# Kernel optimization log

Hardware: AMD Instinct MI355X
Metric: run time of the kernel (lower is better)

The kernel has to match this reference:

```python
import jax, jax.numpy as jnp
import numpy as np

N_PROTS, D = 20000, 256
N_NODES, N_EDGES = 100000, 320000
N_GRAPHS, OUT = 64, 978
EPS = 1e-5


def setup_inputs() -> dict:
    key = jax.random.key(0)
    ks = jax.random.split(key, 24)
    f = jax.random.normal
    inp = {
        'global_idx': jax.random.randint(ks[0], (N_NODES,), 0, N_PROTS),
        'acts': f(ks[1], (N_NODES, 2), dtype=jnp.float32),
        'edge_index': jax.random.randint(ks[2], (2, N_EDGES), 0, N_NODES),
        'sign': f(ks[3], (N_EDGES, 2), dtype=jnp.float32),
        'batch': jnp.sort(jax.random.randint(ks[4], (N_NODES,), 0, N_GRAPHS)),
        # parameters
        'emb_weight': f(ks[5], (N_PROTS, D)) * 0.02,
        'pe_W': f(ks[6], (2, D)) * 0.02,
        'pe_b': jnp.zeros((D,)),
        'cg_Wf': f(ks[7], (2 * D + 2, D)) * 0.02,
        'cg_bf': jnp.zeros((D,)),
        'cg_Ws': f(ks[8], (2 * D + 2, D)) * 0.02,
        'cg_bs': jnp.zeros((D,)),
        'gat_W': f(ks[9], (4, D, D)) * 0.05,
        'gat_att_src': f(ks[10], (4, D)) * 0.05,
        'gat_att_dst': f(ks[11], (4, D)) * 0.05,
        'gat_bias': jnp.zeros((4, D)),
        'bn_gamma': jnp.ones((5, D)),
        'bn_beta': jnp.zeros((5, D)),
        'prelu_alpha': jnp.full((5,), 0.25),
        'fc1_W': f(ks[12], (D, 2 * D)) * 0.02,
        'fc1_b': jnp.zeros((2 * D,)),
        'fc2_W': f(ks[13], (2 * D, OUT)) * 0.02,
        'fc2_b': jnp.zeros((OUT,)),
    }
    return inp


def _bn(h, gamma, beta):
    # eval-mode BatchNorm1d with running_mean=0, running_var=1
    return h / jnp.sqrt(1.0 + EPS) * gamma + beta


def _prelu(h, a):
    return jnp.where(h >= 0, h, a * h)


def _cgconv(x, src, dst, sign, Wf, bf, Ws, bs):
    # PyG CGConv: z = [x_i, x_j, e_ij]; out = x + sum_j sigmoid(lin_f(z)) * softplus(lin_s(z))
    z = jnp.concatenate([x[dst], x[src], sign], axis=-1)  # [E, 2D+2]
    msg = jax.nn.sigmoid(z @ Wf + bf) * jax.nn.softplus(z @ Ws + bs)
    return x + jax.ops.segment_sum(msg, dst, num_segments=x.shape[0])


def _gat(x, src_sl, dst_sl, W, a_src, a_dst, b):
    # PyG GATConv, heads=1, self-loops already appended to src_sl/dst_sl
    N = x.shape[0]
    h = x @ W                                  # [N, D]
    asrc = h @ a_src                           # [N]
    adst = h @ a_dst                           # [N]
    logit = jax.nn.leaky_relu(asrc[src_sl] + adst[dst_sl], 0.2)  # [E+N]
    m = jax.ops.segment_max(logit, dst_sl, num_segments=N)
    ex = jnp.exp(logit - m[dst_sl])
    denom = jax.ops.segment_sum(ex, dst_sl, num_segments=N)
    coef = ex / denom[dst_sl]
    out = jax.ops.segment_sum(h[src_sl] * coef[:, None], dst_sl, num_segments=N)
    return out + b


def reference(global_idx, acts, edge_index, sign, batch, emb_weight, pe_W, pe_b,
              cg_Wf, cg_bf, cg_Ws, cg_bs, gat_W, gat_att_src, gat_att_dst,
              gat_bias, bn_gamma, bn_beta, prelu_alpha, fc1_W, fc1_b, fc2_W, fc2_b):
    N = global_idx.shape[0]
    src, dst = edge_index[0], edge_index[1]
    loop = jnp.arange(N)
    src_sl = jnp.concatenate([src, loop])
    dst_sl = jnp.concatenate([dst, loop])

    x = emb_weight[global_idx] + (acts @ pe_W + pe_b)

    h = _cgconv(x, src, dst, sign, cg_Wf, cg_bf, cg_Ws, cg_bs)
    h = _prelu(_bn(h, bn_gamma[0], bn_beta[0]) + x, prelu_alpha[0])

    for l in range(4):
        g = _gat(h, src_sl, dst_sl, gat_W[l], gat_att_src[l], gat_att_dst[l], gat_bias[l])
        h = _prelu(_bn(g, bn_gamma[l + 1], bn_beta[l + 1]) + h, prelu_alpha[l + 1])

    # NOTE: original code pools the *input* features x (x is never reassigned
    # to x_5 before pooling) -- reproduced faithfully.
    pooled = jax.ops.segment_sum(x, batch, num_segments=N_GRAPHS)  # [G, D]
    z = jax.nn.relu(pooled @ fc1_W + fc1_b)
    return jax.nn.log_softmax(z @ fc2_W + fc2_b, axis=-1)
```

## Files before the change

kernel.cpp:

```cpp
#include <hip/hip_runtime.h>


#define NNODES  100000
#define NGRAPHS 64
#define DIM     256
#define HID     512
#define NOUT    978
#define NPW     32

__global__ __launch_bounds__(256) void pool_k(
    const int* __restrict__ gidx, const float* __restrict__ acts,
    const int* __restrict__ batch, const float* __restrict__ emb,
    const float* __restrict__ peW, const float* __restrict__ peb,
    float* __restrict__ pooled)
{
    const int wave = blockIdx.x * 4 + (threadIdx.x >> 6);
    const int lane = threadIdx.x & 63;
    const int start = wave * NPW;
    if (start >= NNODES) return;

    const float4 w0 = ((const float4*)peW)[lane];
    const float4 w1 = ((const float4*)(peW + DIM))[lane];
    const float4 pb = ((const float4*)peb)[lane];

    float4 acc  = make_float4(0.f, 0.f, 0.f, 0.f);
    float2 asum = make_float2(0.f, 0.f);
    float  cnt  = 0.f;
    int cur = batch[start];

    auto flush = [&]() {
        float* p = pooled + (size_t)cur * DIM + lane * 4;
        atomicAdd(p + 0, acc.x + asum.x * w0.x + asum.y * w1.x + cnt * pb.x);
        atomicAdd(p + 1, acc.y + asum.x * w0.y + asum.y * w1.y + cnt * pb.y);
        atomicAdd(p + 2, acc.z + asum.x * w0.z + asum.y * w1.z + cnt * pb.z);
        atomicAdd(p + 3, acc.w + asum.x * w0.w + asum.y * w1.w + cnt * pb.w);
        acc = make_float4(0.f, 0.f, 0.f, 0.f);
        asum = make_float2(0.f, 0.f);
        cnt = 0.f;
    };

    #pragma unroll
    for (int t = 0; t < NPW / 8; ++t) {
        const int i = start + t * 8;
        const int4 b0 = *(const int4*)(batch + i);
        const int4 b1 = *(const int4*)(batch + i + 4);
        const int4 p0 = *(const int4*)(gidx + i);
        const int4 p1 = *(const int4*)(gidx + i + 4);
        const float4 a0 = *(const float4*)(acts + 2 * i);
        const float4 a1 = *(const float4*)(acts + 2 * i + 4);
        const float4 a2 = *(const float4*)(acts + 2 * i + 8);
        const float4 a3 = *(const float4*)(acts + 2 * i + 12);
        const float4 e0 = *(const float4*)(emb + ((size_t)p0.x << 8) + lane * 4);
        const float4 e1 = *(const float4*)(emb + ((size_t)p0.y << 8) + lane * 4);
        const float4 e2 = *(const float4*)(emb + ((size_t)p0.z << 8) + lane * 4);
        const float4 e3 = *(const float4*)(emb + ((size_t)p0.w << 8) + lane * 4);
        const float4 e4 = *(const float4*)(emb + ((size_t)p1.x << 8) + lane * 4);
        const float4 e5 = *(const float4*)(emb + ((size_t)p1.y << 8) + lane * 4);
        const float4 e6 = *(const float4*)(emb + ((size_t)p1.z << 8) + lane * 4);
        const float4 e7 = *(const float4*)(emb + ((size_t)p1.w << 8) + lane * 4);

        if (b1.w == cur) {
            acc.x += (e0.x + e1.x) + (e2.x + e3.x) + (e4.x + e5.x) + (e6.x + e7.x);
            acc.y += (e0.y + e1.y) + (e2.y + e3.y) + (e4.y + e5.y) + (e6.y + e7.y);
            acc.z += (e0.z + e1.z) + (e2.z + e3.z) + (e4.z + e5.z) + (e6.z + e7.z);
            acc.w += (e0.w + e1.w) + (e2.w + e3.w) + (e4.w + e5.w) + (e6.w + e7.w);
            asum.x += (a0.x + a0.z) + (a1.x + a1.z) + (a2.x + a2.z) + (a3.x + a3.z);
            asum.y += (a0.y + a0.w) + (a1.y + a1.w) + (a2.y + a2.w) + (a3.y + a3.w);
            cnt += 8.f;
        } else {
#define NODE(B, E, AX, AY) do {                                   \
            if ((B) != cur) { flush(); cur = (B); }               \
            acc.x += (E).x; acc.y += (E).y;                       \
            acc.z += (E).z; acc.w += (E).w;                       \
            asum.x += (AX); asum.y += (AY); cnt += 1.f; } while (0)
            NODE(b0.x, e0, a0.x, a0.y);
            NODE(b0.y, e1, a0.z, a0.w);
            NODE(b0.z, e2, a1.x, a1.y);
            NODE(b0.w, e3, a1.z, a1.w);
            NODE(b1.x, e4, a2.x, a2.y);
            NODE(b1.y, e5, a2.z, a2.w);
            NODE(b1.z, e6, a3.x, a3.y);
            NODE(b1.w, e7, a3.z, a3.w);
#undef NODE
        }
    }
    flush();
}

__global__ __launch_bounds__(256) void fc1_k(
    const float* __restrict__ pooled, const float* __restrict__ W,
    const float* __restrict__ bias, float* __restrict__ z)
{
    __shared__ float xs[DIM];
    const int g = blockIdx.y;
    const int j = blockIdx.x * 256 + threadIdx.x;
    xs[threadIdx.x] = pooled[g * DIM + threadIdx.x];
    __syncthreads();

    float acc = bias[j];
#pragma unroll 4
    for (int d = 0; d < DIM; d += 4) {
        const float4 x4 = *(const float4*)(xs + d);
        acc = fmaf(x4.x, W[(d + 0) * HID + j], acc);
        acc = fmaf(x4.y, W[(d + 1) * HID + j], acc);
        acc = fmaf(x4.z, W[(d + 2) * HID + j], acc);
        acc = fmaf(x4.w, W[(d + 3) * HID + j], acc);
    }
    z[g * HID + j] = fmaxf(acc, 0.f);
}

__global__ __launch_bounds__(256) void fc2_k(
    const float* __restrict__ z, const float* __restrict__ W,
    const float* __restrict__ bias, float* __restrict__ out)
{
    __shared__ float zs[2 * HID];
    const int g0 = blockIdx.y * 2;
    const int j = blockIdx.x * 256 + threadIdx.x;
#pragma unroll
    for (int k = 0; k < 4; ++k) {
        const int idx = threadIdx.x + k * 256;
        zs[idx] = z[g0 * HID + idx];
    }
    __syncthreads();
    if (j >= NOUT) return;

    float acc0 = bias[j], acc1 = acc0;
#pragma unroll 2
    for (int d = 0; d < HID; d += 4) {
        const float4 za = *(const float4*)(zs + d);
        const float4 zb = *(const float4*)(zs + HID + d);
        const float wa = W[(d + 0) * NOUT + j];
        const float wb = W[(d + 1) * NOUT + j];
        const float wc = W[(d + 2) * NOUT + j];
        const float wd = W[(d + 3) * NOUT + j];
        acc0 = fmaf(za.x, wa, acc0); acc1 = fmaf(zb.x, wa, acc1);
        acc0 = fmaf(za.y, wb, acc0); acc1 = fmaf(zb.y, wb, acc1);
        acc0 = fmaf(za.z, wc, acc0); acc1 = fmaf(zb.z, wc, acc1);
        acc0 = fmaf(za.w, wd, acc0); acc1 = fmaf(zb.w, wd, acc1);
    }
    out[(size_t)g0 * NOUT + j]       = acc0;
    out[(size_t)(g0 + 1) * NOUT + j] = acc1;
}

__global__ __launch_bounds__(256) void lsm_k(float* __restrict__ out)
{
    __shared__ float red[8];
    const int g = blockIdx.x;
    float* row = out + (size_t)g * NOUT;
    const int tid  = threadIdx.x;
    const int wid  = tid >> 6;
    const int lane = tid & 63;

    float v[4];
    float m = -INFINITY;
#pragma unroll
    for (int k = 0; k < 4; ++k) {
        const int j = tid + k * 256;
        v[k] = (j < NOUT) ? row[j] : -INFINITY;
        m = fmaxf(m, v[k]);
    }
#pragma unroll
    for (int off = 32; off > 0; off >>= 1) m = fmaxf(m, __shfl_xor(m, off));
    if (lane == 0) red[wid] = m;
    __syncthreads();
    m = fmaxf(fmaxf(red[0], red[1]), fmaxf(red[2], red[3]));

    float s = 0.f;
#pragma unroll
    for (int k = 0; k < 4; ++k) {
        const int j = tid + k * 256;
        if (j < NOUT) s += expf(v[k] - m);
    }
#pragma unroll
    for (int off = 32; off > 0; off >>= 1) s += __shfl_xor(s, off);
    if (lane == 0) red[4 + wid] = s;
    __syncthreads();
    s = red[4] + red[5] + red[6] + red[7];

    const float lse = m + logf(s);
#pragma unroll
    for (int k = 0; k < 4; ++k) {
        const int j = tid + k * 256;
        if (j < NOUT) row[j] = v[k] - lse;
    }
}

extern "C" void kernel_launch(void* const* d_in, const int* in_sizes, int n_in,
                              void* d_out, int out_size, void* d_ws, size_t ws_size,
                              hipStream_t stream)
{
    const int*   gidx  = (const int*)  d_in[0];
    const float* acts  = (const float*)d_in[1];
    const int*   batch = (const int*)  d_in[4];
    const float* emb   = (const float*)d_in[5];
    const float* peW   = (const float*)d_in[6];
    const float* peb   = (const float*)d_in[7];
    const float* fc1W  = (const float*)d_in[19];
    const float* fc1b  = (const float*)d_in[20];
    const float* fc2W  = (const float*)d_in[21];
    const float* fc2b  = (const float*)d_in[22];

    float* pooled = (float*)d_ws;
    float* z      = pooled + NGRAPHS * DIM;

    hipMemsetAsync(pooled, 0, NGRAPHS * DIM * sizeof(float), stream);

    const int waves  = (NNODES + NPW - 1) / NPW;
    const int blocks = (waves + 3) / 4;
    pool_k<<<blocks, 256, 0, stream>>>(gidx, acts, batch, emb, peW, peb, pooled);
    fc1_k<<<dim3(2, NGRAPHS), 256, 0, stream>>>(pooled, fc1W, fc1b, z);
    fc2_k<<<dim3(4, NGRAPHS / 2), 256, 0, stream>>>(z, fc2W, fc2b, (float*)d_out);
    lsm_k<<<NGRAPHS, 256, 0, stream>>>((float*)d_out);
}
```

Baseline: 74.20 us.

## Halve nodes per wave, issue all gathers upfront, widen fc2 graphs per block

The pooling kernel now gives each wave 16 nodes instead of 32 and issues all index, activation and embedding-row loads before any accumulation, so more memory requests are in flight. The old multi-iteration loop is gone. fc2 now computes four graphs per block so each weight load is reused more, and the hipMemsetAsync is replaced by a small zeroing kernel. The cost is roughly twice as many pool waves and atomic flushes, and fewer fc2 blocks.

```diff
diff --git a/kernel.cpp b/kernel.cpp
--- a/kernel.cpp
+++ b/kernel.cpp
@@ -6,7 +6,12 @@
 #define DIM     256
 #define HID     512
 #define NOUT    978
-#define NPW     32
+#define NPW     16
+
+__global__ __launch_bounds__(256) void zero_k(float4* __restrict__ p)
+{
+    p[blockIdx.x * 256 + threadIdx.x] = make_float4(0.f, 0.f, 0.f, 0.f);
+}
 
 __global__ __launch_bounds__(256) void pool_k(
     const int* __restrict__ gidx, const float* __restrict__ acts,
@@ -16,17 +21,41 @@
 {
     const int wave = blockIdx.x * 4 + (threadIdx.x >> 6);
     const int lane = threadIdx.x & 63;
-    const int start = wave * NPW;
-    if (start >= NNODES) return;
+    const int i = wave * NPW;
+    if (i >= NNODES) return;
 
     const float4 w0 = ((const float4*)peW)[lane];
     const float4 w1 = ((const float4*)(peW + DIM))[lane];
     const float4 pb = ((const float4*)peb)[lane];
 
+    const int4 b0 = *(const int4*)(batch + i);
+    const int4 b1 = *(const int4*)(batch + i + 4);
+    const int4 b2 = *(const int4*)(batch + i + 8);
+    const int4 b3 = *(const int4*)(batch + i + 12);
+    const int4 p0 = *(const int4*)(gidx + i);
+    const int4 p1 = *(const int4*)(gidx + i + 4);
+    const int4 p2 = *(const int4*)(gidx + i + 8);
+    const int4 p3 = *(const int4*)(gidx + i + 12);
+    const float4 a0 = *(const float4*)(acts + 2 * i);
+    const float4 a1 = *(const float4*)(acts + 2 * i + 4);
+    const float4 a2 = *(const float4*)(acts + 2 * i + 8);
+    const float4 a3 = *(const float4*)(acts + 2 * i + 12);
+    const float4 a4 = *(const float4*)(acts + 2 * i + 16);
+    const float4 a5 = *(const float4*)(acts + 2 * i + 20);
+    const float4 a6 = *(const float4*)(acts + 2 * i + 24);
+    const float4 a7 = *(const float4*)(acts + 2 * i + 28);
+
+#define EROW(P) (*(const float4*)(emb + ((size_t)(P) << 8) + lane * 4))
+    const float4 e0 = EROW(p0.x), e1 = EROW(p0.y), e2 = EROW(p0.z), e3 = EROW(p0.w);
+    const float4 e4 = EROW(p1.x), e5 = EROW(p1.y), e6 = EROW(p1.z), e7 = EROW(p1.w);
+    const float4 e8 = EROW(p2.x), e9 = EROW(p2.y), eA = EROW(p2.z), eB = EROW(p2.w);
+    const float4 eC = EROW(p3.x), eD = EROW(p3.y), eE = EROW(p3.z), eF = EROW(p3.w);
+#undef EROW
+
     float4 acc  = make_float4(0.f, 0.f, 0.f, 0.f);
     float2 asum = make_float2(0.f, 0.f);
     float  cnt  = 0.f;
-    int cur = batch[start];
+    int cur = b0.x;
 
     auto flush = [&]() {
         float* p = pooled + (size_t)cur * DIM + lane * 4;
@@ -39,52 +68,46 @@
         cnt = 0.f;
     };
 
-    #pragma unroll
-    for (int t = 0; t < NPW / 8; ++t) {
-        const int i = start + t * 8;
-        const int4 b0 = *(const int4*)(batch + i);
-        const int4 b1 = *(const int4*)(batch + i + 4);
-        const int4 p0 = *(const int4*)(gidx + i);
-        const int4 p1 = *(const int4*)(gidx + i + 4);
-        const float4 a0 = *(const float4*)(acts + 2 * i);
-        const float4 a1 = *(const float4*)(acts + 2 * i + 4);
-        const float4 a2 = *(const float4*)(acts + 2 * i + 8);
-        const float4 a3 = *(const float4*)(acts + 2 * i + 12);
-        const float4 e0 = *(const float4*)(emb + ((size_t)p0.x << 8) + lane * 4);
-        const float4 e1 = *(const float4*)(emb + ((size_t)p0.y << 8) + lane * 4);
-        const float4 e2 = *(const float4*)(emb + ((size_t)p0.z << 8) + lane * 4);
-        const float4 e3 = *(const float4*)(emb + ((size_t)p0.w << 8) + lane * 4);
-        const float4 e4 = *(const float4*)(emb + ((size_t)p1.x << 8) + lane * 4);
-        const float4 e5 = *(const float4*)(emb + ((size_t)p1.y << 8) + lane * 4);
-        const float4 e6 = *(const float4*)(emb + ((size_t)p1.z << 8) + lane * 4);
-        const float4 e7 = *(const float4*)(emb + ((size_t)p1.w << 8) + lane * 4);
-
-        if (b1.w == cur) {
-            acc.x += (e0.x + e1.x) + (e2.x + e3.x) + (e4.x + e5.x) + (e6.x + e7.x);
-            acc.y += (e0.y + e1.y) + (e2.y + e3.y) + (e4.y + e5.y) + (e6.y + e7.y);
-            acc.z += (e0.z + e1.z) + (e2.z + e3.z) + (e4.z + e5.z) + (e6.z + e7.z);
-            acc.w += (e0.w + e1.w) + (e2.w + e3.w) + (e4.w + e5.w) + (e6.w + e7.w);
-            asum.x += (a0.x + a0.z) + (a1.x + a1.z) + (a2.x + a2.z) + (a3.x + a3.z);
-            asum.y += (a0.y + a0.w) + (a1.y + a1.w) + (a2.y + a2.w) + (a3.y + a3.w);
-            cnt += 8.f;
-        } else {
+    if (b3.w == cur) {
+        acc.x = (((e0.x + e1.x) + (e2.x + e3.x)) + ((e4.x + e5.x) + (e6.x + e7.x)))
+              + (((e8.x + e9.x) + (eA.x + eB.x)) + ((eC.x + eD.x) + (eE.x + eF.x)));
+        acc.y = (((e0.y + e1.y) + (e2.y + e3.y)) + ((e4.y + e5.y) + (e6.y + e7.y)))
+              + (((e8.y + e9.y) + (eA.y + eB.y)) + ((eC.y + eD.y) + (eE.y + eF.y)));
+        acc.z = (((e0.z + e1.z) + (e2.z + e3.z)) + ((e4.z + e5.z) + (e6.z + e7.z)))
+              + (((e8.z + e9.z) + (eA.z + eB.z)) + ((eC.z + eD.z) + (eE.z + eF.z)));
+        acc.w = (((e0.w + e1.w) + (e2.w + e3.w)) + ((e4.w + e5.w) + (e6.w + e7.w)))
+              + (((e8.w + e9.w) + (eA.w + eB.w)) + ((eC.w + eD.w) + (eE.w + eF.w)));
+        asum.x = ((a0.x + a0.z) + (a1.x + a1.z)) + ((a2.x + a2.z) + (a3.x + a3.z))
+               + ((a4.x + a4.z) + (a5.x + a5.z)) + ((a6.x + a6.z) + (a7.x + a7.z));
+        asum.y = ((a0.y + a0.w) + (a1.y + a1.w)) + ((a2.y + a2.w) + (a3.y + a3.w))
+               + ((a4.y + a4.w) + (a5.y + a5.w)) + ((a6.y + a6.w) + (a7.y + a7.w));
+        cnt = 16.f;
+        flush();
+    } else {
 #define NODE(B, E, AX, AY) do {                                   \
-            if ((B) != cur) { flush(); cur = (B); }               \
-            acc.x += (E).x; acc.y += (E).y;                       \
-            acc.z += (E).z; acc.w += (E).w;                       \
-            asum.x += (AX); asum.y += (AY); cnt += 1.f; } while (0)
-            NODE(b0.x, e0, a0.x, a0.y);
-            NODE(b0.y, e1, a0.z, a0.w);
-            NODE(b0.z, e2, a1.x, a1.y);
-            NODE(b0.w, e3, a1.z, a1.w);
-            NODE(b1.x, e4, a2.x, a2.y);
-            NODE(b1.y, e5, a2.z, a2.w);
-            NODE(b1.z, e6, a3.x, a3.y);
-            NODE(b1.w, e7, a3.z, a3.w);
+        if ((B) != cur) { flush(); cur = (B); }                   \
+        acc.x += (E).x; acc.y += (E).y;                           \
+        acc.z += (E).z; acc.w += (E).w;                           \
+        asum.x += (AX); asum.y += (AY); cnt += 1.f; } while (0)
+        NODE(b0.x, e0, a0.x, a0.y);
+        NODE(b0.y, e1, a0.z, a0.w);
+        NODE(b0.z, e2, a1.x, a1.y);
+        NODE(b0.w, e3, a1.z, a1.w);
+        NODE(b1.x, e4, a2.x, a2.y);
+        NODE(b1.y, e5, a2.z, a2.w);
+        NODE(b1.z, e6, a3.x, a3.y);
+        NODE(b1.w, e7, a3.z, a3.w);
+        NODE(b2.x, e8, a4.x, a4.y);
+        NODE(b2.y, e9, a4.z, a4.w);
+        NODE(b2.z, eA, a5.x, a5.y);
+        NODE(b2.w, eB, a5.z, a5.w);
+        NODE(b3.x, eC, a6.x, a6.y);
+        NODE(b3.y, eD, a6.z, a6.w);
+        NODE(b3.z, eE, a7.x, a7.y);
+        NODE(b3.w, eF, a7.z, a7.w);
 #undef NODE
-        }
-    }
-    flush();
+        flush();
+    }
 }
 
 __global__ __launch_bounds__(256) void fc1_k(
@@ -113,33 +136,41 @@
     const float* __restrict__ z, const float* __restrict__ W,
     const float* __restrict__ bias, float* __restrict__ out)
 {
-    __shared__ float zs[2 * HID];
-    const int g0 = blockIdx.y * 2;
+    __shared__ float zs[4 * HID];
+    const int g0 = blockIdx.y * 4;
     const int j = blockIdx.x * 256 + threadIdx.x;
 #pragma unroll
-    for (int k = 0; k < 4; ++k) {
+    for (int k = 0; k < 8; ++k) {
         const int idx = threadIdx.x + k * 256;
         zs[idx] = z[g0 * HID + idx];
     }
     __syncthreads();
     if (j >= NOUT) return;
 
-    float acc0 = bias[j], acc1 = acc0;
+    float acc0 = bias[j], acc1 = acc0, acc2 = acc0, acc3 = acc0;
 #pragma unroll 2
     for (int d = 0; d < HID; d += 4) {
         const float4 za = *(const float4*)(zs + d);
         const float4 zb = *(const float4*)(zs + HID + d);
+        const float4 zc = *(const float4*)(zs + 2 * HID + d);
+        const float4 zd = *(const float4*)(zs + 3 * HID + d);
         const float wa = W[(d + 0) * NOUT + j];
         const float wb = W[(d + 1) * NOUT + j];
         const float wc = W[(d + 2) * NOUT + j];
         const float wd = W[(d + 3) * NOUT + j];
         acc0 = fmaf(za.x, wa, acc0); acc1 = fmaf(zb.x, wa, acc1);
+        acc2 = fmaf(zc.x, wa, acc2); acc3 = fmaf(zd.x, wa, acc3);
         acc0 = fmaf(za.y, wb, acc0); acc1 = fmaf(zb.y, wb, acc1);
+        acc2 = fmaf(zc.y, wb, acc2); acc3 = fmaf(zd.y, wb, acc3);
         acc0 = fmaf(za.z, wc, acc0); acc1 = fmaf(zb.z, wc, acc1);
+        acc2 = fmaf(zc.z, wc, acc2); acc3 = fmaf(zd.z, wc, acc3);
         acc0 = fmaf(za.w, wd, acc0); acc1 = fmaf(zb.w, wd, acc1);
-    }
-    out[(size_t)g0 * NOUT + j]       = acc0;
+        acc2 = fmaf(zc.w, wd, acc2); acc3 = fmaf(zd.w, wd, acc3);
+    }
+    out[(size_t)(g0 + 0) * NOUT + j] = acc0;
     out[(size_t)(g0 + 1) * NOUT + j] = acc1;
+    out[(size_t)(g0 + 2) * NOUT + j] = acc2;
+    out[(size_t)(g0 + 3) * NOUT + j] = acc3;
 }
 
 __global__ __launch_bounds__(256) void lsm_k(float* __restrict__ out)
@@ -203,12 +234,12 @@
     float* pooled = (float*)d_ws;
     float* z      = pooled + NGRAPHS * DIM;
 
-    hipMemsetAsync(pooled, 0, NGRAPHS * DIM * sizeof(float), stream);
+    zero_k<<<16, 256, 0, stream>>>((float4*)pooled);
 
     const int waves  = (NNODES + NPW - 1) / NPW;
     const int blocks = (waves + 3) / 4;
     pool_k<<<blocks, 256, 0, stream>>>(gidx, acts, batch, emb, peW, peb, pooled);
     fc1_k<<<dim3(2, NGRAPHS), 256, 0, stream>>>(pooled, fc1W, fc1b, z);
-    fc2_k<<<dim3(4, NGRAPHS / 2), 256, 0, stream>>>(z, fc2W, fc2b, (float*)d_out);
+    fc2_k<<<dim3(4, NGRAPHS / 4), 256, 0, stream>>>(z, fc2W, fc2b, (float*)d_out);
     lsm_k<<<NGRAPHS, 256, 0, stream>>>((float*)d_out);
 }
```

Result: slower. 95.67 us (+28.9%).
